# Kernel optimization log

Measured on AMD Instinct MI355X. Metric: run time of the kernel, lower is better.

The kernel has to match this reference:

```python
import jax, jax.numpy as jnp
import numpy as np

D_MODEL = 1024
N_REG = 8
D_REG = 32
LN_EPS = 1e-5


def setup_inputs() -> dict:
    key = jax.random.key(0)
    ks = jax.random.split(key, 14)
    s = 0.02
    return {
        "x": jax.random.normal(ks[0], (8, 2048, D_MODEL), dtype=jnp.float32),
        "ln_w": jnp.ones((D_MODEL,), jnp.float32),
        "ln_b": jnp.zeros((D_MODEL,), jnp.float32),
        "Wrq": jax.random.normal(ks[1], (N_REG, D_MODEL), jnp.float32) * s,
        "brq": jax.random.normal(ks[2], (N_REG,), jnp.float32) * s,
        "Wrp": jax.random.normal(ks[3], (D_MODEL, D_REG), jnp.float32) * s,
        "brp": jax.random.normal(ks[4], (D_MODEL,), jnp.float32) * s,
        "Wwq": jax.random.normal(ks[5], (N_REG, D_MODEL), jnp.float32) * s,
        "bwq": jax.random.normal(ks[6], (N_REG,), jnp.float32) * s,
        "Wwv": jax.random.normal(ks[7], (D_REG, D_MODEL), jnp.float32) * s,
        "bwv": jax.random.normal(ks[8], (D_REG,), jnp.float32) * s,
        "Wwg": jax.random.normal(ks[9], (1, D_MODEL), jnp.float32) * s,
        "bwg": jnp.full((1,), -3.0, jnp.float32),
        "mix": jnp.asarray(0.001, jnp.float32),
    }


def _layernorm(x, w, b):
    mu = jnp.mean(x, axis=-1, keepdims=True)
    var = jnp.mean(jnp.square(x - mu), axis=-1, keepdims=True)
    return (x - mu) * jax.lax.rsqrt(var + LN_EPS) * w + b


def _forward(x, ln_w, ln_b, Wrq, brq, Wrp, brp, Wwq, bwq, Wwv, bwv, Wwg, bwg, mix):
    B, L, D = x.shape
    h = _layernorm(x, ln_w, ln_b)  # (B,L,D)
    # Precompute all per-timestep projections as big GEMMs (same math as per-step Linear)
    r_w = jax.nn.softmax(jnp.einsum("bld,rd->blr", h, Wrq) + brq, axis=-1)  # (B,L,R)
    w_w = jax.nn.softmax(jnp.einsum("bld,rd->blr", h, Wwq) + bwq, axis=-1)  # (B,L,R)
    w_v = jnp.einsum("bld,kd->blk", h, Wwv) + bwv                           # (B,L,Dr)
    w_g = jax.nn.sigmoid(jnp.einsum("bld,od->blo", h, Wwg) + bwg)           # (B,L,1)

    def step(registers, inputs):
        rw_t, ww_t, wv_t, wg_t = inputs  # (B,R), (B,R), (B,Dr), (B,1)
        r_v = jnp.einsum("br,brd->bd", rw_t, registers)  # read (B,Dr)
        us = (ww_t * wg_t)[..., None]                     # (B,R,1)
        new_regs = (1.0 - us) * registers + us * wv_t[:, None, :]
        return new_regs, r_v

    init_regs = jnp.zeros((B, N_REG, D_REG), x.dtype)
    seq = (
        jnp.moveaxis(r_w, 1, 0),
        jnp.moveaxis(w_w, 1, 0),
        jnp.moveaxis(w_v, 1, 0),
        jnp.moveaxis(w_g, 1, 0),
    )
    _, r_vs = jax.lax.scan(step, init_regs, seq)  # (L,B,Dr)
    r_vs = jnp.moveaxis(r_vs, 0, 1)               # (B,L,Dr)
    r_out = jnp.einsum("blk,dk->bld", r_vs, Wrp) + brp  # read_proj
    return mix * r_out


def reference(x, ln_w, ln_b, Wrq, brq, Wrp, brp, Wwq, bwq, Wwv, bwv, Wwg, bwg, mix):
    return _forward(x, ln_w, ln_b, Wrq, brq, Wrp, brp, Wwq, bwq, Wwv, bwv, Wwg, bwg, mix)
```

## Files before the change

kernel.cpp:

```cpp
#include <hip/hip_runtime.h>

#define D_MODEL 1024
#define L_SEQ   2048
#define N_BATCH 8
#define N_TOK   (N_BATCH * L_SEQ)
#define N_REGS  8
#define D_REG   32
#define LN_EPS  1e-5f

#define HSTEP   16
#define N_HALF  128

#define ASTR    36
#define ABUF    (64 * ASTR)
#define BUFSZ   (4 * ABUF)
#define OFF_AH  0
#define OFF_AL  ABUF
#define OFF_BH  (2 * ABUF)
#define OFF_BL  (3 * ABUF)
#define OFF_SB  (2 * BUFSZ)
#define SBSTR   68
#define OFF_PH  (OFF_SB + 64 * SBSTR)
#define OFF_PS  (OFF_PH + 64 * 17)
#define LDS_DW  (OFF_PS + 64 * 17)

typedef short short8v __attribute__((ext_vector_type(8)));
typedef short short4v __attribute__((ext_vector_type(4)));
typedef float float4v __attribute__((ext_vector_type(4)));

__device__ __forceinline__ float wred(float v) {
    #pragma unroll
    for (int off = 32; off > 0; off >>= 1) v += __shfl_xor(v, off, 64);
    return v;
}

__device__ __forceinline__ float sigmoidf(float z) {
    return 1.f / (1.f + expf(-z));
}

__device__ __forceinline__ unsigned short f2bf(float f) {
    unsigned u = __float_as_uint(f);
    return (unsigned short)((u + 0x7FFFu + ((u >> 16) & 1u)) >> 16);
}
__device__ __forceinline__ float bf2f(unsigned short h) {
    return __uint_as_float(((unsigned)h) << 16);
}

__global__ __launch_bounds__(256) void k_prep2(
    const float* __restrict__ ln_w, const float* __restrict__ ln_b,
    const float* __restrict__ Wrq,  const float* __restrict__ brq,
    const float* __restrict__ Wwq,  const float* __restrict__ bwq,
    const float* __restrict__ Wwv,  const float* __restrict__ bwv,
    const float* __restrict__ Wwg,  const float* __restrict__ bwg,
    unsigned short* __restrict__ Wbh, unsigned short* __restrict__ Wbl,
    float* __restrict__ c1, float* __restrict__ c2)
{
    const int f = blockIdx.x;

    const float* wrow = nullptr; float bias = 0.f;
    if (f < 8)        { wrow = Wrq + f * D_MODEL;        bias = brq[f]; }
    else if (f < 16)  { wrow = Wwq + (f - 8) * D_MODEL;  bias = bwq[f - 8]; }
    else if (f == 16) { wrow = Wwg;                      bias = bwg[0]; }
    else if (f < 49)  { wrow = Wwv + (f - 17) * D_MODEL; bias = bwv[f - 17]; }

    float p1 = 0.f, p2 = 0.f;
    #pragma unroll
    for (int j = 0; j < 4; ++j) {
        const int k = j * 256 + threadIdx.x;
        float w  = wrow ? wrow[k] : 0.f;
        float wp = w * ln_w[k];
        unsigned short h = f2bf(wp);
        unsigned short l = f2bf(wp - bf2f(h));
        Wbh[(size_t)f * D_MODEL + k] = h;
        Wbl[(size_t)f * D_MODEL + k] = l;
        p1 += wp;
        p2 = fmaf(w, ln_b[k], p2);
    }
    p1 = wred(p1); p2 = wred(p2);

    __shared__ float r1[4], r2[4];
    const int l = threadIdx.x & 63, w = threadIdx.x >> 6;
    if (l == 0) { r1[w] = p1; r2[w] = p2; }
    __syncthreads();
    if (threadIdx.x == 0) {
        c1[f] = r1[0] + r1[1] + r1[2] + r1[3];
        c2[f] = r2[0] + r2[1] + r2[2] + r2[3] + bias;
    }
}

__device__ __forceinline__ void cvt_write_a(
    float* lds, int wb, int stok, int skq, float4 v, float& ssum, float& ssq)
{
    unsigned short h0 = f2bf(v.x), h1 = f2bf(v.y), h2 = f2bf(v.z), h3 = f2bf(v.w);
    short4v hv, lv;
    hv[0] = (short)h0; hv[1] = (short)h1; hv[2] = (short)h2; hv[3] = (short)h3;
    lv[0] = (short)f2bf(v.x - bf2f(h0));
    lv[1] = (short)f2bf(v.y - bf2f(h1));
    lv[2] = (short)f2bf(v.z - bf2f(h2));
    lv[3] = (short)f2bf(v.w - bf2f(h3));
    *reinterpret_cast<short4v*>(lds + wb + OFF_AH + stok * ASTR + skq * 2) = hv;
    *reinterpret_cast<short4v*>(lds + wb + OFF_AL + stok * ASTR + skq * 2) = lv;
    ssum += v.x + v.y + v.z + v.w;
    ssq = fmaf(v.x, v.x, fmaf(v.y, v.y, fmaf(v.z, v.z, fmaf(v.w, v.w, ssq))));
}

__global__ __launch_bounds__(1024) void k_lnmfma(
    const float* __restrict__ x,
    const uint4* __restrict__ Wbh, const uint4* __restrict__ Wbl,
    const float* __restrict__ c1, const float* __restrict__ c2,
    float* __restrict__ rw_o, float* __restrict__ us_o, float* __restrict__ wv_o)
{
    extern __shared__ float lds[];

    const int tid  = threadIdx.x;
    const int lane = tid & 63;
    const int wv   = tid >> 6;
    const int tt   = wv >> 2;
    const int ft   = wv & 3;
    const int tok0 = blockIdx.x * 64;

    const int stok = tid >> 4;
    const int skq  = tid & 15;
    const float4* xg4 = reinterpret_cast<const float4*>(x) + (size_t)(tok0 + stok) * 256;
    const uint4*  wsrc = (skq < 8 ? Wbh : Wbl) + (size_t)stok * 128;
    const int     wkq  = skq & 7;
    const int     wdst = (skq < 8 ? OFF_BH : OFF_BL) + stok * ASTR + wkq * 4;

    float ssum = 0.f, ssq = 0.f;
    float4 xg = xg4[skq];
    uint4  bg = wsrc[wkq];

    cvt_write_a(lds, 0, stok, skq, xg, ssum, ssq);
    *reinterpret_cast<uint4*>(lds + wdst) = bg;
    __syncthreads();

    float4v acc = {0.f, 0.f, 0.f, 0.f};
    const int m = lane & 15, oct = lane >> 4;
    const int arow = (tt * 16 + m) * ASTR + oct * 4;
    const int brow = (ft * 16 + m) * ASTR + oct * 4;

    for (int c = 0; c < 16; ++c) {
        if (c < 15) {
            xg = xg4[(c + 1) * 16 + skq];
            bg = wsrc[(c + 1) * 8 + wkq];
        }
        const int bb = (c & 1) * BUFSZ;
        #pragma unroll
        for (int ks = 0; ks < 2; ++ks) {
            const int ao = bb + arow + ks * 16;
            const int bo = bb + brow + ks * 16;
            short8v ah = *reinterpret_cast<const short8v*>(lds + OFF_AH + ao);
            short8v al = *reinterpret_cast<const short8v*>(lds + OFF_AL + ao);
            short8v bh = *reinterpret_cast<const short8v*>(lds + OFF_BH + bo);
            short8v bl = *reinterpret_cast<const short8v*>(lds + OFF_BL + bo);
            acc = __builtin_amdgcn_mfma_f32_16x16x32_bf16(ah, bh, acc, 0, 0, 0);
            acc = __builtin_amdgcn_mfma_f32_16x16x32_bf16(ah, bl, acc, 0, 0, 0);
            acc = __builtin_amdgcn_mfma_f32_16x16x32_bf16(al, bh, acc, 0, 0, 0);
        }
        if (c < 15) {
            const int wb = ((c + 1) & 1) * BUFSZ;
            cvt_write_a(lds, wb, stok, skq, xg, ssum, ssq);
            *reinterpret_cast<uint4*>(lds + wb + wdst) = bg;
        }
        __syncthreads();
    }

    lds[OFF_PH + stok * 17 + skq] = ssum;
    lds[OFF_PS + stok * 17 + skq] = ssq;
    {
        const int row0 = tt * 16 + oct * 4;
        const int col  = ft * 16 + m;
        #pragma unroll
        for (int r = 0; r < 4; ++r)
            lds[OFF_SB + (row0 + r) * SBSTR + col] = acc[r];
    }
    __syncthreads();

    if (tid < 64) {
        float s = 0.f, q = 0.f;
        #pragma unroll
        for (int i = 0; i < 16; ++i) {
            s += lds[OFF_PH + tid * 17 + i];
            q += lds[OFF_PS + tid * 17 + i];
        }
        lds[OFF_SB + tid * SBSTR + 50] = s;
        lds[OFF_SB + tid * SBSTR + 51] = q;
    }
    __syncthreads();

    if (tid < 256) {
        const int t  = tid & 63;
        const int q  = tid >> 6;
        const int tg = blockIdx.x * 64 + t;
        const float* St = lds + OFF_SB + t * SBSTR;

        const float tsum = St[50], tss = St[51];
        const float mu  = tsum * (1.f / D_MODEL);
        const float var = tss * (1.f / D_MODEL) - mu * mu;
        const float rs  = rsqrtf(var + LN_EPS);

        if (q == 0) {
            float lg[8];
            #pragma unroll
            for (int r = 0; r < 8; ++r)
                lg[r] = rs * (St[r] - mu * c1[r]) + c2[r];
            float mx = lg[0];
            #pragma unroll
            for (int r = 1; r < 8; ++r) mx = fmaxf(mx, lg[r]);
            float sm = 0.f;
            #pragma unroll
            for (int r = 0; r < 8; ++r) { lg[r] = expf(lg[r] - mx); sm += lg[r]; }
            float inv = 1.f / sm;
            float4* o = reinterpret_cast<float4*>(rw_o + (size_t)tg * 8);
            o[0] = make_float4(lg[0]*inv, lg[1]*inv, lg[2]*inv, lg[3]*inv);
            o[1] = make_float4(lg[4]*inv, lg[5]*inv, lg[6]*inv, lg[7]*inv);
        } else if (q == 1) {
            float lg[8];
            #pragma unroll
            for (int r = 0; r < 8; ++r)
                lg[r] = rs * (St[8 + r] - mu * c1[8 + r]) + c2[8 + r];
            float gl = rs * (St[16] - mu * c1[16]) + c2[16];
            float mx = lg[0];
            #pragma unroll
            for (int r = 1; r < 8; ++r) mx = fmaxf(mx, lg[r]);
            float sm = 0.f;
            #pragma unroll
            for (int r = 0; r < 8; ++r) { lg[r] = expf(lg[r] - mx); sm += lg[r]; }
            float inv = sigmoidf(gl) / sm;
            float4* o = reinterpret_cast<float4*>(us_o + (size_t)tg * 8);
            o[0] = make_float4(lg[0]*inv, lg[1]*inv, lg[2]*inv, lg[3]*inv);
            o[1] = make_float4(lg[4]*inv, lg[5]*inv, lg[6]*inv, lg[7]*inv);
        } else {
            const int f0 = 17 + (q - 2) * 16;
            float4* o = reinterpret_cast<float4*>(wv_o + (size_t)tg * 32 + (q - 2) * 16);
            #pragma unroll
            for (int jq = 0; jq < 4; ++jq) {
                float v0 = rs * (St[f0 + jq*4 + 0] - mu * c1[f0 + jq*4 + 0]) + c2[f0 + jq*4 + 0];
                float v1 = rs * (St[f0 + jq*4 + 1] - mu * c1[f0 + jq*4 + 1]) + c2[f0 + jq*4 + 1];
                float v2 = rs * (St[f0 + jq*4 + 2] - mu * c1[f0 + jq*4 + 2]) + c2[f0 + jq*4 + 2];
                float v3 = rs * (St[f0 + jq*4 + 3] - mu * c1[f0 + jq*4 + 3]) + c2[f0 + jq*4 + 3];
                o[jq] = make_float4(v0, v1, v2, v3);
            }
        }
    }
}

__global__ __launch_bounds__(1024) void k_scan(
    const float* __restrict__ us, const float* __restrict__ wv,
    float* __restrict__ S0)
{
    __shared__ float S_us[L_SEQ];
    __shared__ float lA[N_HALF];
    __shared__ float lB[N_HALF * 32];

    const int tid = threadIdx.x;
    const int b   = blockIdx.x >> 3;
    const int r   = blockIdx.x & 7;

    #pragma unroll
    for (int i = 0; i < 2; ++i) {
        const int t = i * 1024 + tid;
        S_us[t] = us[((size_t)(b * L_SEQ + t)) * 8 + r];
    }
    __syncthreads();

    const int k  = tid & 31;
    const int hb = (tid >> 5) * 4;
    #pragma unroll
    for (int j = 0; j < 4; ++j) {
        const int h  = hb + j;
        const int t0 = h * HSTEP;
        const float* wvp = wv + ((size_t)(b * L_SEQ + t0)) * 32 + k;

        float Aacc = 1.f, Bacc = 0.f;
        #pragma unroll
        for (int gq = 0; gq < 2; ++gq) {
            float wl[8], ul[8];
            #pragma unroll
            for (int e = 0; e < 8; ++e) {
                wl[e] = wvp[(gq * 8 + e) * 32];
                ul[e] = S_us[t0 + gq * 8 + e];
            }
            #pragma unroll
            for (int e = 0; e < 8; ++e) {
                float a = 1.f - ul[e];
                Aacc *= a;
                Bacc = fmaf(a, Bacc, ul[e] * wl[e]);
            }
        }
        lB[h * 32 + k] = Bacc;
        if (k == 0) lA[h] = Aacc;
    }
    __syncthreads();

    if (tid < 32) {
        float stv = 0.f;
        float* S0p = S0 + ((size_t)(b * 8 + r) * N_HALF) * 32 + tid;
        for (int h = 0; h < N_HALF; ++h) {
            S0p[h * 32] = stv;
            stv = fmaf(lA[h], stv, lB[h * 32 + tid]);
        }
    }
}

__global__ __launch_bounds__(256) void k_replay2(
    const float* __restrict__ rw, const float* __restrict__ us,
    const float* __restrict__ wv, const float* __restrict__ S0,
    float* __restrict__ rvs)
{
    const int gid = blockIdx.x * 256 + threadIdx.x;
    const int k   = gid & 31;
    const int hu  = gid >> 5;
    const int b   = hu >> 7;
    const int ch2 = hu & 127;

    float s[8];
    #pragma unroll
    for (int r = 0; r < 8; ++r)
        s[r] = S0[((size_t)((b * 8 + r) * N_HALF) + ch2) * 32 + k];

    const int t0 = b * L_SEQ + ch2 * HSTEP;
    const float* rwp = rw + (size_t)t0 * 8;
    const float* usp = us + (size_t)t0 * 8;
    const float* wvp = wv + (size_t)t0 * 32 + k;
    float*       rvp = rvs + (size_t)t0 * 32 + k;

    #pragma unroll
    for (int g4 = 0; g4 < 4; ++g4) {
        float4 r0[4], r1[4], u0[4], u1[4];
        float  wl[4];
        #pragma unroll
        for (int j = 0; j < 4; ++j) {
            const int t = g4 * 4 + j;
            r0[j] = reinterpret_cast<const float4*>(rwp + t * 8)[0];
            r1[j] = reinterpret_cast<const float4*>(rwp + t * 8)[1];
            u0[j] = reinterpret_cast<const float4*>(usp + t * 8)[0];
            u1[j] = reinterpret_cast<const float4*>(usp + t * 8)[1];
            wl[j] = wvp[t * 32];
        }
        #pragma unroll
        for (int j = 0; j < 4; ++j) {
            const int t = g4 * 4 + j;
            float rv = r0[j].x*s[0] + r0[j].y*s[1] + r0[j].z*s[2] + r0[j].w*s[3]
                     + r1[j].x*s[4] + r1[j].y*s[5] + r1[j].z*s[6] + r1[j].w*s[7];
            rvp[t * 32] = rv;
            const float w = wl[j];
            s[0] = fmaf(u0[j].x, w - s[0], s[0]);
            s[1] = fmaf(u0[j].y, w - s[1], s[1]);
            s[2] = fmaf(u0[j].z, w - s[2], s[2]);
            s[3] = fmaf(u0[j].w, w - s[3], s[3]);
            s[4] = fmaf(u1[j].x, w - s[4], s[4]);
            s[5] = fmaf(u1[j].y, w - s[5], s[5]);
            s[6] = fmaf(u1[j].z, w - s[6], s[6]);
            s[7] = fmaf(u1[j].w, w - s[7], s[7]);
        }
    }
}

__global__ __launch_bounds__(256) void k_outproj(
    const float* __restrict__ rvs, const float* __restrict__ Wrp,
    const float* __restrict__ brp, const float* __restrict__ mix_p,
    float* __restrict__ out)
{
    const int d    = blockIdx.y * 256 + threadIdx.x;
    const int tok0 = blockIdx.x * 64;

    float4 wr[8];
    #pragma unroll
    for (int q = 0; q < 8; ++q)
        wr[q] = reinterpret_cast<const float4*>(Wrp)[(size_t)d * 8 + q];

    const float bias = brp[d];
    const float mix  = mix_p[0];

    for (int t = 0; t < 64; ++t) {
        const float4* rv = reinterpret_cast<const float4*>(rvs + (size_t)(tok0 + t) * 32);
        float acc = 0.f;
        #pragma unroll
        for (int q = 0; q < 8; ++q) {
            float4 v = rv[q];
            acc += wr[q].x*v.x + wr[q].y*v.y + wr[q].z*v.z + wr[q].w*v.w;
        }
        out[(size_t)(tok0 + t) * D_MODEL + d] = mix * (acc + bias);
    }
}

extern "C" void kernel_launch(void* const* d_in, const int* in_sizes, int n_in,
                              void* d_out, int out_size, void* d_ws, size_t ws_size,
                              hipStream_t stream)
{
    const float* x    = (const float*)d_in[0];
    const float* ln_w = (const float*)d_in[1];
    const float* ln_b = (const float*)d_in[2];
    const float* Wrq  = (const float*)d_in[3];
    const float* brq  = (const float*)d_in[4];
    const float* Wrp  = (const float*)d_in[5];
    const float* brp  = (const float*)d_in[6];
    const float* Wwq  = (const float*)d_in[7];
    const float* bwq  = (const float*)d_in[8];
    const float* Wwv  = (const float*)d_in[9];
    const float* bwv  = (const float*)d_in[10];
    const float* Wwg  = (const float*)d_in[11];
    const float* bwg  = (const float*)d_in[12];
    const float* mix  = (const float*)d_in[13];
    float* out = (float*)d_out;

    float* ws   = (float*)d_ws;
    float* rw_b = ws;
    float* us_b = ws + 131072;
    float* wv_b = ws + 262144;
    float* S0_b = ws + 786432;
    float* rv_b = ws + 1048576;
    unsigned short* Wbh = (unsigned short*)rv_b;
    unsigned short* Wbl = (unsigned short*)(rv_b + 32768);
    float* c1_b = rv_b + 65536;
    float* c2_b = rv_b + 65600;

    k_prep2<<<64, 256, 0, stream>>>(ln_w, ln_b, Wrq, brq, Wwq, bwq,
                                    Wwv, bwv, Wwg, bwg, Wbh, Wbl, c1_b, c2_b);
    k_lnmfma<<<256, 1024, LDS_DW * 4, stream>>>(
        x, (const uint4*)Wbh, (const uint4*)Wbl, c1_b, c2_b, rw_b, us_b, wv_b);
    k_scan   <<<64, 1024, 0, stream>>>(us_b, wv_b, S0_b);
    k_replay2<<<128, 256, 0, stream>>>(rw_b, us_b, wv_b, S0_b, rv_b);
    dim3 gc(N_TOK / 64, 4);
    k_outproj<<<gc, 256, 0, stream>>>(rv_b, Wrp, brp, mix, out);
}
```

Measured before the change: 85.42 us.

## Load MFMA fragments straight from global memory and drop LDS staging

The weight prep kernel now writes bf16 hi/lo weights already arranged in MFMA fragment order. The projection kernel then loads x and weight fragments directly into registers with software prefetch, with no double-buffered LDS staging or per-chunk barriers. Blocks are now 512 threads covering 32 tokens, twice as many blocks as before. Each x element is loaded and converted to hi/lo by all four feature-tile waves, which adds redundant global traffic (mostly served from cache) in exchange for no LDS traffic and no synchronisation in the main loop.

```diff
diff --git a/kernel.cpp b/kernel.cpp
--- a/kernel.cpp
+++ b/kernel.cpp
@@ -11,21 +11,9 @@
 #define HSTEP   16
 #define N_HALF  128
 
-#define ASTR    36
-#define ABUF    (64 * ASTR)
-#define BUFSZ   (4 * ABUF)
-#define OFF_AH  0
-#define OFF_AL  ABUF
-#define OFF_BH  (2 * ABUF)
-#define OFF_BL  (3 * ABUF)
-#define OFF_SB  (2 * BUFSZ)
-#define SBSTR   68
-#define OFF_PH  (OFF_SB + 64 * SBSTR)
-#define OFF_PS  (OFF_PH + 64 * 17)
-#define LDS_DW  (OFF_PS + 64 * 17)
+#define SSTR2   67
 
 typedef short short8v __attribute__((ext_vector_type(8)));
-typedef short short4v __attribute__((ext_vector_type(4)));
 typedef float float4v __attribute__((ext_vector_type(4)));
 
 __device__ __forceinline__ float wred(float v) {
@@ -46,16 +34,16 @@
     return __uint_as_float(((unsigned)h) << 16);
 }
 
-__global__ __launch_bounds__(256) void k_prep2(
+__global__ __launch_bounds__(256) void k_prep3(
     const float* __restrict__ ln_w, const float* __restrict__ ln_b,
     const float* __restrict__ Wrq,  const float* __restrict__ brq,
     const float* __restrict__ Wwq,  const float* __restrict__ bwq,
     const float* __restrict__ Wwv,  const float* __restrict__ bwv,
     const float* __restrict__ Wwg,  const float* __restrict__ bwg,
-    unsigned short* __restrict__ Wbh, unsigned short* __restrict__ Wbl,
-    float* __restrict__ c1, float* __restrict__ c2)
-{
-    const int f = blockIdx.x;
+    unsigned short* __restrict__ Wfrag, float* __restrict__ c1, float* __restrict__ c2)
+{
+    const int f  = blockIdx.x;
+    const int ft = f >> 4, fm = f & 15;
 
     const float* wrow = nullptr; float bias = 0.f;
     if (f < 8)        { wrow = Wrq + f * D_MODEL;        bias = brq[f]; }
@@ -65,14 +53,17 @@
 
     float p1 = 0.f, p2 = 0.f;
     #pragma unroll
-    for (int j = 0; j < 4; ++j) {
-        const int k = j * 256 + threadIdx.x;
+    for (int j2 = 0; j2 < 4; ++j2) {
+        const int k = j2 * 256 + threadIdx.x;
         float w  = wrow ? wrow[k] : 0.f;
         float wp = w * ln_w[k];
         unsigned short h = f2bf(wp);
         unsigned short l = f2bf(wp - bf2f(h));
-        Wbh[(size_t)f * D_MODEL + k] = h;
-        Wbl[(size_t)f * D_MODEL + k] = l;
+        const int c = k >> 5, oct = (k >> 3) & 3, j = k & 7;
+        const int lane = (oct << 4) | fm;
+        const size_t base = ((((size_t)c * 4 + ft) * 2) * 64 + lane) * 8 + j;
+        Wfrag[base]       = h;
+        Wfrag[base + 512] = l;
         p1 += wp;
         p2 = fmaf(w, ln_b[k], p2);
     }
@@ -88,113 +79,96 @@
     }
 }
 
-__device__ __forceinline__ void cvt_write_a(
-    float* lds, int wb, int stok, int skq, float4 v, float& ssum, float& ssq)
-{
-    unsigned short h0 = f2bf(v.x), h1 = f2bf(v.y), h2 = f2bf(v.z), h3 = f2bf(v.w);
-    short4v hv, lv;
-    hv[0] = (short)h0; hv[1] = (short)h1; hv[2] = (short)h2; hv[3] = (short)h3;
-    lv[0] = (short)f2bf(v.x - bf2f(h0));
-    lv[1] = (short)f2bf(v.y - bf2f(h1));
-    lv[2] = (short)f2bf(v.z - bf2f(h2));
-    lv[3] = (short)f2bf(v.w - bf2f(h3));
-    *reinterpret_cast<short4v*>(lds + wb + OFF_AH + stok * ASTR + skq * 2) = hv;
-    *reinterpret_cast<short4v*>(lds + wb + OFF_AL + stok * ASTR + skq * 2) = lv;
-    ssum += v.x + v.y + v.z + v.w;
-    ssq = fmaf(v.x, v.x, fmaf(v.y, v.y, fmaf(v.z, v.z, fmaf(v.w, v.w, ssq))));
-}
-
-__global__ __launch_bounds__(1024) void k_lnmfma(
-    const float* __restrict__ x,
-    const uint4* __restrict__ Wbh, const uint4* __restrict__ Wbl,
+__global__ __launch_bounds__(512) void k_lnmfma2(
+    const float* __restrict__ x, const uint4* __restrict__ Wfrag,
     const float* __restrict__ c1, const float* __restrict__ c2,
     float* __restrict__ rw_o, float* __restrict__ us_o, float* __restrict__ wv_o)
 {
-    extern __shared__ float lds[];
+    __shared__ float Sb[32 * SSTR2];
 
     const int tid  = threadIdx.x;
     const int lane = tid & 63;
     const int wv   = tid >> 6;
-    const int tt   = wv >> 2;
+    const int mt   = wv >> 2;
     const int ft   = wv & 3;
-    const int tok0 = blockIdx.x * 64;
-
-    const int stok = tid >> 4;
-    const int skq  = tid & 15;
-    const float4* xg4 = reinterpret_cast<const float4*>(x) + (size_t)(tok0 + stok) * 256;
-    const uint4*  wsrc = (skq < 8 ? Wbh : Wbl) + (size_t)stok * 128;
-    const int     wkq  = skq & 7;
-    const int     wdst = (skq < 8 ? OFF_BH : OFF_BL) + stok * ASTR + wkq * 4;
-
+    const int m = lane & 15, oct = lane >> 4;
+    const int tok0 = blockIdx.x * 32;
+    const int tok  = tok0 + mt * 16 + m;
+
+    const float4* xp = reinterpret_cast<const float4*>(x + (size_t)tok * D_MODEL) + oct * 2;
+    const uint4*  bp = Wfrag + (size_t)(ft * 2) * 64 + lane;
+
+    float4v acc = {0.f, 0.f, 0.f, 0.f};
     float ssum = 0.f, ssq = 0.f;
-    float4 xg = xg4[skq];
-    uint4  bg = wsrc[wkq];
-
-    cvt_write_a(lds, 0, stok, skq, xg, ssum, ssq);
-    *reinterpret_cast<uint4*>(lds + wdst) = bg;
-    __syncthreads();
-
-    float4v acc = {0.f, 0.f, 0.f, 0.f};
-    const int m = lane & 15, oct = lane >> 4;
-    const int arow = (tt * 16 + m) * ASTR + oct * 4;
-    const int brow = (ft * 16 + m) * ASTR + oct * 4;
-
-    for (int c = 0; c < 16; ++c) {
-        if (c < 15) {
-            xg = xg4[(c + 1) * 16 + skq];
-            bg = wsrc[(c + 1) * 8 + wkq];
-        }
-        const int bb = (c & 1) * BUFSZ;
-        #pragma unroll
-        for (int ks = 0; ks < 2; ++ks) {
-            const int ao = bb + arow + ks * 16;
-            const int bo = bb + brow + ks * 16;
-            short8v ah = *reinterpret_cast<const short8v*>(lds + OFF_AH + ao);
-            short8v al = *reinterpret_cast<const short8v*>(lds + OFF_AL + ao);
-            short8v bh = *reinterpret_cast<const short8v*>(lds + OFF_BH + bo);
-            short8v bl = *reinterpret_cast<const short8v*>(lds + OFF_BL + bo);
-            acc = __builtin_amdgcn_mfma_f32_16x16x32_bf16(ah, bh, acc, 0, 0, 0);
-            acc = __builtin_amdgcn_mfma_f32_16x16x32_bf16(ah, bl, acc, 0, 0, 0);
-            acc = __builtin_amdgcn_mfma_f32_16x16x32_bf16(al, bh, acc, 0, 0, 0);
-        }
-        if (c < 15) {
-            const int wb = ((c + 1) & 1) * BUFSZ;
-            cvt_write_a(lds, wb, stok, skq, xg, ssum, ssq);
-            *reinterpret_cast<uint4*>(lds + wb + wdst) = bg;
-        }
-        __syncthreads();
-    }
-
-    lds[OFF_PH + stok * 17 + skq] = ssum;
-    lds[OFF_PS + stok * 17 + skq] = ssq;
+
+    float4 xa = xp[0], xb = xp[1];
+    uint4  vbh = bp[0], vbl = bp[64];
+
+    #pragma unroll 2
+    for (int c = 0; c < 32; ++c) {
+        float4 nxa, nxb; uint4 nbh, nbl;
+        if (c < 31) {
+            nxa = xp[(c + 1) * 8];
+            nxb = xp[(c + 1) * 8 + 1];
+            nbh = bp[(c + 1) * 512];
+            nbl = bp[(c + 1) * 512 + 64];
+        }
+
+        short8v ah, al;
+        {
+            const float v0 = xa.x, v1 = xa.y, v2 = xa.z, v3 = xa.w;
+            const float v4 = xb.x, v5 = xb.y, v6 = xb.z, v7 = xb.w;
+            unsigned short h;
+            h = f2bf(v0); ah[0] = (short)h; al[0] = (short)f2bf(v0 - bf2f(h));
+            h = f2bf(v1); ah[1] = (short)h; al[1] = (short)f2bf(v1 - bf2f(h));
+            h = f2bf(v2); ah[2] = (short)h; al[2] = (short)f2bf(v2 - bf2f(h));
+            h = f2bf(v3); ah[3] = (short)h; al[3] = (short)f2bf(v3 - bf2f(h));
+            h = f2bf(v4); ah[4] = (short)h; al[4] = (short)f2bf(v4 - bf2f(h));
+            h = f2bf(v5); ah[5] = (short)h; al[5] = (short)f2bf(v5 - bf2f(h));
+            h = f2bf(v6); ah[6] = (short)h; al[6] = (short)f2bf(v6 - bf2f(h));
+            h = f2bf(v7); ah[7] = (short)h; al[7] = (short)f2bf(v7 - bf2f(h));
+            if (ft == 0) {
+                ssum += ((v0 + v1) + (v2 + v3)) + ((v4 + v5) + (v6 + v7));
+                ssq = fmaf(v0, v0, ssq); ssq = fmaf(v1, v1, ssq);
+                ssq = fmaf(v2, v2, ssq); ssq = fmaf(v3, v3, ssq);
+                ssq = fmaf(v4, v4, ssq); ssq = fmaf(v5, v5, ssq);
+                ssq = fmaf(v6, v6, ssq); ssq = fmaf(v7, v7, ssq);
+            }
+        }
+
+        short8v bh = __builtin_bit_cast(short8v, vbh);
+        short8v bl = __builtin_bit_cast(short8v, vbl);
+        acc = __builtin_amdgcn_mfma_f32_16x16x32_bf16(ah, bh, acc, 0, 0, 0);
+        acc = __builtin_amdgcn_mfma_f32_16x16x32_bf16(ah, bl, acc, 0, 0, 0);
+        acc = __builtin_amdgcn_mfma_f32_16x16x32_bf16(al, bh, acc, 0, 0, 0);
+
+        xa = nxa; xb = nxb; vbh = nbh; vbl = nbl;
+    }
+
+    if (ft == 0) {
+        ssum += __shfl_xor(ssum, 16, 64); ssq += __shfl_xor(ssq, 16, 64);
+        ssum += __shfl_xor(ssum, 32, 64); ssq += __shfl_xor(ssq, 32, 64);
+        if (oct == 0) {
+            Sb[(mt * 16 + m) * SSTR2 + 64] = ssum;
+            Sb[(mt * 16 + m) * SSTR2 + 65] = ssq;
+        }
+    }
     {
-        const int row0 = tt * 16 + oct * 4;
+        const int row0 = mt * 16 + oct * 4;
         const int col  = ft * 16 + m;
         #pragma unroll
         for (int r = 0; r < 4; ++r)
-            lds[OFF_SB + (row0 + r) * SBSTR + col] = acc[r];
+            Sb[(row0 + r) * SSTR2 + col] = acc[r];
     }
     __syncthreads();
 
-    if (tid < 64) {
-        float s = 0.f, q = 0.f;
-        #pragma unroll
-        for (int i = 0; i < 16; ++i) {
-            s += lds[OFF_PH + tid * 17 + i];
-            q += lds[OFF_PS + tid * 17 + i];
-        }
-        lds[OFF_SB + tid * SBSTR + 50] = s;
-        lds[OFF_SB + tid * SBSTR + 51] = q;
-    }
-    __syncthreads();
-
-    if (tid < 256) {
-        const int t  = tid & 63;
-        const int q  = tid >> 6;
-        const int tg = blockIdx.x * 64 + t;
-        const float* St = lds + OFF_SB + t * SBSTR;
-
-        const float tsum = St[50], tss = St[51];
+    if (tid < 128) {
+        const int t  = tid & 31;
+        const int q  = tid >> 5;
+        const int tg = tok0 + t;
+        const float* St = Sb + t * SSTR2;
+
+        const float tsum = St[64], tss = St[65];
         const float mu  = tsum * (1.f / D_MODEL);
         const float var = tss * (1.f / D_MODEL) - mu * mu;
         const float rs  = rsqrtf(var + LN_EPS);
@@ -411,15 +385,14 @@
     float* wv_b = ws + 262144;
     float* S0_b = ws + 786432;
     float* rv_b = ws + 1048576;
-    unsigned short* Wbh = (unsigned short*)rv_b;
-    unsigned short* Wbl = (unsigned short*)(rv_b + 32768);
+    unsigned short* Wfrag = (unsigned short*)rv_b;
     float* c1_b = rv_b + 65536;
     float* c2_b = rv_b + 65600;
 
-    k_prep2<<<64, 256, 0, stream>>>(ln_w, ln_b, Wrq, brq, Wwq, bwq,
-                                    Wwv, bwv, Wwg, bwg, Wbh, Wbl, c1_b, c2_b);
-    k_lnmfma<<<256, 1024, LDS_DW * 4, stream>>>(
-        x, (const uint4*)Wbh, (const uint4*)Wbl, c1_b, c2_b, rw_b, us_b, wv_b);
+    k_prep3<<<64, 256, 0, stream>>>(ln_w, ln_b, Wrq, brq, Wwq, bwq,
+                                    Wwv, bwv, Wwg, bwg, Wfrag, c1_b, c2_b);
+    k_lnmfma2<<<512, 512, 0, stream>>>(
+        x, (const uint4*)Wfrag, c1_b, c2_b, rw_b, us_b, wv_b);
     k_scan   <<<64, 1024, 0, stream>>>(us_b, wv_b, S0_b);
     k_replay2<<<128, 256, 0, stream>>>(rw_b, us_b, wv_b, S0_b, rv_b);
     dim3 gc(N_TOK / 64, 4);
```

Measured after the change: 86.65 us. About the same (+1.4%).
